# Optimization experiments

Hardware: AMD Instinct MI355X
Metric: run time of the kernel (lower is better)

The kernel has to match this reference:

```python
import jax, jax.numpy as jnp
import numpy as np
from math import sqrt

MASK_SCALE = 128  # band half-width; entries with |i-j| < MASK_SCALE are masked to -inf

B, L, H, E = 4, 2048, 8, 64
D = 64


def setup_inputs() -> dict:
    key = jax.random.key(0)
    kq, kk, kv = jax.random.split(key, 3)
    queries = jax.random.normal(kq, (B, L, H, E), dtype=jnp.float32)
    keys = jax.random.normal(kk, (B, L, H, E), dtype=jnp.float32)
    values = jax.random.normal(kv, (B, L, H, D), dtype=jnp.float32)
    attn_mask = jnp.zeros((B, 1, L, L), dtype=bool)  # unused (mask_flag=False)
    return {"queries": queries, "keys": keys, "values": values, "attn_mask": attn_mask}


def reference(queries, keys, values, attn_mask):
    b, l, h, e = queries.shape
    scale = 1.0 / sqrt(e)
    # [B,H,L,S] dense scores
    scores = jnp.einsum('blhe,bshe->bhls', queries, keys)
    # create_diag_symmetric_mask(L, MASK_SCALE): 1 iff |i-j| < MASK_SCALE
    idx = jnp.arange(l)
    band = jnp.abs(idx[:, None] - idx[None, :]) < MASK_SCALE  # [L,L]
    # module masks the band to -inf (attends outside the band)
    scores = jnp.where(band[None, None, :, :], -jnp.inf, scores)
    A = jax.nn.softmax(scale * scores, axis=-1)
    V = jnp.einsum('bhls,bshd->blhd', A, values)
    return V
```

## Files before the change

### kernel.cpp

```cpp
#include <hip/hip_runtime.h>
#include <hip/hip_bf16.h>

typedef __bf16 bf16_t;
typedef __bf16 bf16x8 __attribute__((ext_vector_type(8)));
typedef float f32x4 __attribute__((ext_vector_type(4)));
typedef float f32x16 __attribute__((ext_vector_type(16)));
typedef unsigned int u32;

#define MFMA16(A,B,C) __builtin_amdgcn_mfma_f32_16x16x32_bf16(A,B,C,0,0,0)
#define MFMA32(A,B,C) __builtin_amdgcn_mfma_f32_32x32x16_bf16(A,B,C,0,0,0)

constexpr int Bb = 4, Ll = 2048, Hh = 8, Ee = 64, Dd = 64;
constexpr int LDP = 72;
constexpr int MS = 128;

static __device__ __forceinline__ bf16x8 cvt8(float4 a, float4 b) {
    bf16x8 t;
    t[0] = (bf16_t)a.x; t[1] = (bf16_t)a.y; t[2] = (bf16_t)a.z; t[3] = (bf16_t)a.w;
    t[4] = (bf16_t)b.x; t[5] = (bf16_t)b.y; t[6] = (bf16_t)b.z; t[7] = (bf16_t)b.w;
    return t;
}

static __device__ __forceinline__ u32 pkbf(float lo, float hi) {
    u32 d;
    asm("v_cvt_pk_bf16_f32 %0, %1, %2" : "=v"(d) : "v"(lo), "v"(hi));
    return d;
}

static __device__ __forceinline__ float fexp2(float x) {
    float r;
    asm("v_exp_f32 %0, %1" : "=v"(r) : "v"(x));
    return r;
}

static __device__ __forceinline__ f32x16 zero16() {
    f32x16 z;
    #pragma unroll
    for (int r = 0; r < 16; ++r) z[r] = 0.f;
    return z;
}

__global__ __launch_bounds__(256) void prep(const float* __restrict__ K,
                                            const float* __restrict__ V,
                                            bf16_t* __restrict__ Kb,
                                            bf16_t* __restrict__ Vt) {
    __shared__ bf16_t VLp[Dd][LDP];
    if (blockIdx.x < 2048) {
        const int c = blockIdx.x * 256 + threadIdx.x;
        const int e0 = (c & 7) * 8;
        const int h  = (c >> 3) & (Hh - 1);
        const int l  = (c >> 6) & (Ll - 1);
        const int b  = c >> 17;
        const float* s = K + ((((size_t)b * Ll + l) * Hh + h) * Ee + e0);
        float4 f0 = ((const float4*)s)[0];
        float4 f1 = ((const float4*)s)[1];
        *(bf16x8*)(Kb + ((((size_t)b * Hh + h) * Ll + l) * Ee + e0)) = cvt8(f0, f1);
    } else {
        const int bb = blockIdx.x - 2048;
        const int bh = bb >> 5;
        const int t  = bb & 31;
        const int b = bh >> 3, h = bh & 7;
        {
            const int j  = threadIdx.x >> 2;
            const int d0 = (threadIdx.x & 3) * 16;
            const float* vp = V + (((size_t)(b * Ll + t * 64 + j)) * Hh + h) * Dd + d0;
            float4 x0 = ((const float4*)vp)[0], x1 = ((const float4*)vp)[1];
            float4 x2 = ((const float4*)vp)[2], x3 = ((const float4*)vp)[3];
            VLp[d0 +  0][j] = (bf16_t)x0.x; VLp[d0 +  1][j] = (bf16_t)x0.y;
            VLp[d0 +  2][j] = (bf16_t)x0.z; VLp[d0 +  3][j] = (bf16_t)x0.w;
            VLp[d0 +  4][j] = (bf16_t)x1.x; VLp[d0 +  5][j] = (bf16_t)x1.y;
            VLp[d0 +  6][j] = (bf16_t)x1.z; VLp[d0 +  7][j] = (bf16_t)x1.w;
            VLp[d0 +  8][j] = (bf16_t)x2.x; VLp[d0 +  9][j] = (bf16_t)x2.y;
            VLp[d0 + 10][j] = (bf16_t)x2.z; VLp[d0 + 11][j] = (bf16_t)x2.w;
            VLp[d0 + 12][j] = (bf16_t)x3.x; VLp[d0 + 13][j] = (bf16_t)x3.y;
            VLp[d0 + 14][j] = (bf16_t)x3.z; VLp[d0 + 15][j] = (bf16_t)x3.w;
        }
        __syncthreads();
        {
            const int d  = threadIdx.x >> 2;
            const int j0 = (threadIdx.x & 3) * 16;
            bf16x8 a0 = *(const bf16x8*)&VLp[d][j0];
            bf16x8 a1 = *(const bf16x8*)&VLp[d][j0 + 8];
            bf16_t* op = Vt + ((((size_t)bh * 32 + t) * 64 + d) * 64 + j0);
            *(bf16x8*)op = a0;
            *(bf16x8*)(op + 8) = a1;
        }
    }
}

__global__ __launch_bounds__(512, 1) void fattn10(const float* __restrict__ Q,
                                                  const bf16_t* __restrict__ Kb,
                                                  const bf16_t* __restrict__ Vt,
                                                  float* __restrict__ O) {
    __shared__ __align__(16) bf16_t KL[2 * 4096];
    __shared__ __align__(16) bf16_t VL[2 * 4096];

    const int tid = threadIdx.x;
    const int wv  = tid >> 6;
    const int ln  = tid & 63;
    const int l31 = ln & 31;
    const int lh  = ln >> 5;

    const int bid = blockIdx.x;
    const int x   = bid & 7;
    const int o   = bid >> 3;
    const int bh  = x * 4 + (o >> 3);
    const int p   = o & 7;
    const int qt  = (wv < 4) ? p : (p + 8);
    const int wq0 = qt * 128 + (wv & 3) * 32;
    const int qq  = wq0 + l31;
    const int b = bh >> 3, h = bh & 7;

    const bf16_t* kbase = Kb + (size_t)bh * (Ll * 64);
    const bf16_t* vbase = Vt + (size_t)bh * (Ll * 64);

    bf16x8 qreg[4];
    {
        const float SCL2 = 0.125f * 1.44269504f;
        const float* qp = Q + (((size_t)(b * Ll + qq)) * Hh + h) * Ee + lh * 8;
        #pragma unroll
        for (int ks = 0; ks < 4; ++ks) {
            float4 f0 = *(const float4*)(qp + ks * 16);
            float4 f1 = *(const float4*)(qp + ks * 16 + 4);
            f0.x *= SCL2; f0.y *= SCL2; f0.z *= SCL2; f0.w *= SCL2;
            f1.x *= SCL2; f1.y *= SCL2; f1.z *= SCL2; f1.w *= SCL2;
            qreg[ks] = cvt8(f0, f1);
        }
    }

    bf16x8 ones;
    #pragma unroll
    for (int e = 0; e < 8; ++e) ones[e] = (bf16_t)1.0f;

    f32x16 acc0 = zero16(), acc1 = zero16(), accP = zero16();

    const int srow = tid >> 3;
    const int soff = srow * 64 + (((tid & 7) ^ (srow & 7)) << 3);
    const int ldst = tid * 8;

    #define STAGE(nxt, kt_) do {                                                   \
        __builtin_amdgcn_global_load_lds((const void*)(kbase + (size_t)(kt_) * 4096\
                                         + soff), (void*)(KL + (nxt) * 4096 + ldst), 16, 0, 0); \
        __builtin_amdgcn_global_load_lds((const void*)(vbase + (size_t)(kt_) * 4096\
                                         + soff), (void*)(VL + (nxt) * 4096 + ldst), 16, 0, 0); \
    } while (0)

    STAGE(0, 0);

    for (int i = 0; i < 32; ++i) {
        const int k0 = i * 64;

        if (i + 1 < 32) {
            STAGE((i + 1) & 1, i + 1);
            asm volatile("s_waitcnt vmcnt(2)" ::: "memory");
        } else {
            asm volatile("s_waitcnt vmcnt(0)" ::: "memory");
        }
        __builtin_amdgcn_s_barrier();

        const int bo = (i & 1) * 4096;

        f32x16 s0v = zero16(), s1v = zero16();
        __builtin_amdgcn_s_setprio(1);
        #pragma unroll
        for (int ks = 0; ks < 4; ++ks) {
            const int cc = (((2 * ks + lh) ^ (l31 & 7)) << 3);
            bf16x8 ka0 = *(const bf16x8*)&KL[bo + l31 * 64 + cc];
            bf16x8 ka1 = *(const bf16x8*)&KL[bo + (32 + l31) * 64 + cc];
            s0v = MFMA32(ka0, qreg[ks], s0v);
            s1v = MFMA32(ka1, qreg[ks], s1v);
        }
        __builtin_amdgcn_s_setprio(0);

        {
            const int d0_ = wq0 - k0;
            if (d0_ > -159 && d0_ < 159) {
                #pragma unroll
                for (int r = 0; r < 16; ++r) {
                    const int k = k0 + 4 * lh + ((r & 3) + 8 * (r >> 2));
                    const int dlt = qq - k;
                    if (dlt > -MS && dlt < MS) s0v[r] = -1e30f;
                }
            }
            const int d1_ = wq0 - (k0 + 32);
            if (d1_ > -159 && d1_ < 159) {
                #pragma unroll
                for (int r = 0; r < 16; ++r) {
                    const int k = k0 + 32 + 4 * lh + ((r & 3) + 8 * (r >> 2));
                    const int dlt = qq - k;
                    if (dlt > -MS && dlt < MS) s1v[r] = -1e30f;
                }
            }
        }

        bf16x8 pf[4];
        {
            float pp[16];
            #pragma unroll
            for (int r = 0; r < 16; ++r) pp[r] = fexp2(s0v[r]);
            u32 x0 = pkbf(pp[0], pp[1]),   x1 = pkbf(pp[2], pp[3]);
            u32 x2 = pkbf(pp[4], pp[5]),   x3 = pkbf(pp[6], pp[7]);
            u32 x4 = pkbf(pp[8], pp[9]),   x5 = pkbf(pp[10], pp[11]);
            u32 x6 = pkbf(pp[12], pp[13]), x7 = pkbf(pp[14], pp[15]);
            asm volatile("v_permlane32_swap_b32 %0, %1" : "+v"(x0), "+v"(x2));
            asm volatile("v_permlane32_swap_b32 %0, %1" : "+v"(x1), "+v"(x3));
            asm volatile("v_permlane32_swap_b32 %0, %1" : "+v"(x4), "+v"(x6));
            asm volatile("v_permlane32_swap_b32 %0, %1" : "+v"(x5), "+v"(x7));
            union { u32 w[4]; bf16x8 v; } u0, u1;
            u0.w[0] = x0; u0.w[1] = x1; u0.w[2] = x2; u0.w[3] = x3;
            u1.w[0] = x4; u1.w[1] = x5; u1.w[2] = x6; u1.w[3] = x7;
            pf[0] = u0.v; pf[1] = u1.v;
        }
        {
            float pp[16];
            #pragma unroll
            for (int r = 0; r < 16; ++r) pp[r] = fexp2(s1v[r]);
            u32 x0 = pkbf(pp[0], pp[1]),   x1 = pkbf(pp[2], pp[3]);
            u32 x2 = pkbf(pp[4], pp[5]),   x3 = pkbf(pp[6], pp[7]);
            u32 x4 = pkbf(pp[8], pp[9]),   x5 = pkbf(pp[10], pp[11]);
            u32 x6 = pkbf(pp[12], pp[13]), x7 = pkbf(pp[14], pp[15]);
            asm volatile("v_permlane32_swap_b32 %0, %1" : "+v"(x0), "+v"(x2));
            asm volatile("v_permlane32_swap_b32 %0, %1" : "+v"(x1), "+v"(x3));
            asm volatile("v_permlane32_swap_b32 %0, %1" : "+v"(x4), "+v"(x6));
            asm volatile("v_permlane32_swap_b32 %0, %1" : "+v"(x5), "+v"(x7));
            union { u32 w[4]; bf16x8 v; } u0, u1;
            u0.w[0] = x0; u0.w[1] = x1; u0.w[2] = x2; u0.w[3] = x3;
            u1.w[0] = x4; u1.w[1] = x5; u1.w[2] = x6; u1.w[3] = x7;
            pf[2] = u0.v; pf[3] = u1.v;
        }

        __builtin_amdgcn_s_setprio(1);
        #pragma unroll
        for (int ks = 0; ks < 4; ++ks) {
            const int cc = (((2 * ks + lh) ^ (l31 & 7)) << 3);
            bf16x8 vf0 = *(const bf16x8*)&VL[bo + l31 * 64 + cc];
            bf16x8 vf1 = *(const bf16x8*)&VL[bo + (32 + l31) * 64 + cc];
            acc0 = MFMA32(pf[ks], vf0, acc0);
            acc1 = MFMA32(pf[ks], vf1, acc1);
            accP = MFMA32(pf[ks], ones, accP);
        }
        __builtin_amdgcn_s_setprio(0);

        __builtin_amdgcn_s_barrier();
    }
    #undef STAGE

    #pragma unroll
    for (int r = 0; r < 16; ++r) {
        const int rr = (r & 3) + 8 * (r >> 2) + 4 * lh;
        const float ir = 1.0f / accP[r];
        float* op = O + ((size_t)(b * Ll + wq0 + rr) * Hh + h) * Dd + l31;
        op[0]  = acc0[r] * ir;
        op[32] = acc1[r] * ir;
    }
}

__global__ __launch_bounds__(256, 2) void fattn_f32(const float* __restrict__ Q,
                                                    const float* __restrict__ K,
                                                    const float* __restrict__ V,
                                                    float* __restrict__ O) {
    __shared__ __align__(16) bf16_t Klds[64][LDP];
    __shared__ __align__(16) bf16_t Vtlds[Dd][LDP];
    __shared__ __align__(16) bf16_t Plds[4][16][LDP];

    const int tid = threadIdx.x;
    const int wv  = tid >> 6;
    const int ln  = tid & 63;
    const int l15 = ln & 15;
    const int g   = ln >> 4;

    const int nqt = Ll / 64;
    const int bid = blockIdx.x;
    const int qt  = bid % nqt;
    const int bh  = bid / nqt;
    const int b   = bh >> 3;
    const int h   = bh & 7;
    const int q0  = qt * 64;

    const float SCL2 = 0.125f * 1.44269504f;

    bf16x8 qf[2];
    {
        const float* qp = Q + (((size_t)(b * Ll + q0 + wv * 16 + l15)) * Hh + h) * Ee + g * 8;
        #pragma unroll
        for (int ks = 0; ks < 2; ++ks) {
            float4 f0 = *(const float4*)(qp + 32 * ks);
            float4 f1 = *(const float4*)(qp + 32 * ks + 4);
            qf[ks] = cvt8(f0, f1);
        }
    }

    f32x4 acc[4];
    #pragma unroll
    for (int ct = 0; ct < 4; ++ct) acc[ct] = (f32x4){0.f, 0.f, 0.f, 0.f};
    float m2[4], lsum[4];
    #pragma unroll
    for (int r = 0; r < 4; ++r) { m2[r] = -1e30f; lsum[r] = 0.f; }

    for (int k0 = 0; k0 < Ll; k0 += 64) {
        const int dd = k0 - q0;
        if (dd >= -64 && dd <= 64) continue;
        const bool needmask = (dd == 128) || (dd == -128);

        __syncthreads();
        {
            const int j  = tid >> 2;
            const int c0 = (tid & 3) << 4;
            const float* kp = K + (((size_t)(b * Ll + k0 + j)) * Hh + h) * Ee + c0;
            const float* vp = V + (((size_t)(b * Ll + k0 + j)) * Hh + h) * Dd + c0;
            float4 a0 = ((const float4*)kp)[0], a1 = ((const float4*)kp)[1];
            float4 a2 = ((const float4*)kp)[2], a3 = ((const float4*)kp)[3];
            *(bf16x8*)&Klds[j][c0]     = cvt8(a0, a1);
            *(bf16x8*)&Klds[j][c0 + 8] = cvt8(a2, a3);
            float4 b0 = ((const float4*)vp)[0], b1 = ((const float4*)vp)[1];
            float4 b2 = ((const float4*)vp)[2], b3 = ((const float4*)vp)[3];
            Vtlds[c0 +  0][j] = (bf16_t)b0.x; Vtlds[c0 +  1][j] = (bf16_t)b0.y;
            Vtlds[c0 +  2][j] = (bf16_t)b0.z; Vtlds[c0 +  3][j] = (bf16_t)b0.w;
            Vtlds[c0 +  4][j] = (bf16_t)b1.x; Vtlds[c0 +  5][j] = (bf16_t)b1.y;
            Vtlds[c0 +  6][j] = (bf16_t)b1.z; Vtlds[c0 +  7][j] = (bf16_t)b1.w;
            Vtlds[c0 +  8][j] = (bf16_t)b2.x; Vtlds[c0 +  9][j] = (bf16_t)b2.y;
            Vtlds[c0 + 10][j] = (bf16_t)b2.z; Vtlds[c0 + 11][j] = (bf16_t)b2.w;
            Vtlds[c0 + 12][j] = (bf16_t)b3.x; Vtlds[c0 + 13][j] = (bf16_t)b3.y;
            Vtlds[c0 + 14][j] = (bf16_t)b3.z; Vtlds[c0 + 15][j] = (bf16_t)b3.w;
        }
        __syncthreads();

        f32x4 s[4];
        #pragma unroll
        for (int ct = 0; ct < 4; ++ct) {
            f32x4 z = (f32x4){0.f, 0.f, 0.f, 0.f};
            #pragma unroll
            for (int ks = 0; ks < 2; ++ks) {
                bf16x8 kf = *(const bf16x8*)&Klds[ct * 16 + l15][ks * 32 + g * 8];
                z = MFMA16(qf[ks], kf, z);
            }
            s[ct] = z;
        }

        float lg[4][4];
        #pragma unroll
        for (int ct = 0; ct < 4; ++ct)
            #pragma unroll
            for (int r = 0; r < 4; ++r)
                lg[ct][r] = s[ct][r] * SCL2;

        if (needmask) {
            const int irow = q0 + wv * 16 + g * 4;
            #pragma unroll
            for (int ct = 0; ct < 4; ++ct) {
                const int j = k0 + ct * 16 + l15;
                #pragma unroll
                for (int r = 0; r < 4; ++r) {
                    int diff = irow + r - j;
                    diff = diff < 0 ? -diff : diff;
                    if (diff < MS) lg[ct][r] = -1e30f;
                }
            }
        }

        #pragma unroll
        for (int r = 0; r < 4; ++r) {
            float mx = fmaxf(fmaxf(lg[0][r], lg[1][r]), fmaxf(lg[2][r], lg[3][r]));
            #pragma unroll
            for (int off = 1; off < 16; off <<= 1) mx = fmaxf(mx, __shfl_xor(mx, off));
            const float mnew = fmaxf(m2[r], mx);
            const float c = exp2f(m2[r] - mnew);
            m2[r] = mnew;
            #pragma unroll
            for (int ct = 0; ct < 4; ++ct) acc[ct][r] *= c;
            float ps = 0.f;
            #pragma unroll
            for (int ct = 0; ct < 4; ++ct) {
                float p = exp2f(lg[ct][r] - mnew);
                bf16_t pb = (bf16_t)p;
                Plds[wv][g * 4 + r][ct * 16 + l15] = pb;
                ps += (float)pb;
            }
            #pragma unroll
            for (int off = 1; off < 16; off <<= 1) ps += __shfl_xor(ps, off);
            lsum[r] = lsum[r] * c + ps;
        }

        __syncthreads();

        #pragma unroll
        for (int ks = 0; ks < 2; ++ks) {
            bf16x8 pfr = *(const bf16x8*)&Plds[wv][l15][ks * 32 + g * 8];
            #pragma unroll
            for (int ct = 0; ct < 4; ++ct) {
                bf16x8 vfl = *(const bf16x8*)&Vtlds[ct * 16 + l15][ks * 32 + g * 8];
                acc[ct] = MFMA16(pfr, vfl, acc[ct]);
            }
        }
    }

    #pragma unroll
    for (int r = 0; r < 4; ++r) {
        const float inv = 1.0f / lsum[r];
        const size_t row = (size_t)(b * Ll + q0 + wv * 16 + g * 4 + r);
        float* op = O + (row * Hh + h) * Dd;
        #pragma unroll
        for (int ct = 0; ct < 4; ++ct)
            op[ct * 16 + l15] = acc[ct][r] * inv;
    }
}

extern "C" void kernel_launch(void* const* d_in, const int* in_sizes, int n_in,
                              void* d_out, int out_size, void* d_ws, size_t ws_size,
                              hipStream_t stream) {
    const float* Q = (const float*)d_in[0];
    const float* K = (const float*)d_in[1];
    const float* V = (const float*)d_in[2];
    float* O = (float*)d_out;

    const size_t nelem = (size_t)Bb * Hh * Ll * Ee;
    const size_t need  = nelem * 2 * 2;

    if (ws_size >= need) {
        bf16_t* Kb = (bf16_t*)d_ws;
        bf16_t* Vt = Kb + nelem;
        prep<<<dim3(3072), dim3(256), 0, stream>>>(K, V, Kb, Vt);
        fattn10<<<dim3(256), dim3(512), 0, stream>>>(Q, Kb, Vt, O);
    } else {
        fattn_f32<<<dim3(Bb * Hh * 32), dim3(256), 0, stream>>>(Q, K, V, O);
    }
}
```

Before: 63.34 us.

## Split key tiles across waves, skip fully masked tiles, reduce partials via LDS

The attention kernel is restructured into 1024 blocks of 256 threads, each owning a 64-query tile. The two wave pairs split each 64-key tile in half and merge their partial outputs and row sums through LDS at the end. Key tiles that fall entirely inside the masked band (up to three per query tile) are skipped. The ones-vector MFMA used for the row sum is replaced by a scalar sum plus a lane shuffle. This raises occupancy and cuts redundant work, at the cost of an extra LDS reduction and barriers.

```diff
diff --git a/kernel.cpp b/kernel.cpp
--- a/kernel.cpp
+++ b/kernel.cpp
@@ -88,33 +88,36 @@
     }
 }
 
-__global__ __launch_bounds__(512, 1) void fattn10(const float* __restrict__ Q,
+__global__ __launch_bounds__(256, 4) void fattn13(const float* __restrict__ Q,
                                                   const bf16_t* __restrict__ Kb,
                                                   const bf16_t* __restrict__ Vt,
                                                   float* __restrict__ O) {
-    __shared__ __align__(16) bf16_t KL[2 * 4096];
-    __shared__ __align__(16) bf16_t VL[2 * 4096];
+    __shared__ __align__(16) bf16_t SMEM[16384];
+    bf16_t* KL = SMEM;
+    bf16_t* VL = SMEM + 8192;
 
     const int tid = threadIdx.x;
     const int wv  = tid >> 6;
     const int ln  = tid & 63;
     const int l31 = ln & 31;
     const int lh  = ln >> 5;
+    const int khalf = wv & 1;
+    const int qhalf = wv >> 1;
 
     const int bid = blockIdx.x;
     const int x   = bid & 7;
     const int o   = bid >> 3;
-    const int bh  = x * 4 + (o >> 3);
-    const int p   = o & 7;
-    const int qt  = (wv < 4) ? p : (p + 8);
-    const int wq0 = qt * 128 + (wv & 3) * 32;
+    const int bh  = x * 4 + (o >> 5);
+    const int qt  = o & 31;
+    const int q0  = qt * 64;
+    const int wq0 = q0 + qhalf * 32;
     const int qq  = wq0 + l31;
     const int b = bh >> 3, h = bh & 7;
 
     const bf16_t* kbase = Kb + (size_t)bh * (Ll * 64);
     const bf16_t* vbase = Vt + (size_t)bh * (Ll * 64);
 
-    bf16x8 qreg[4];
+    bf16x8 qA[4];
     {
         const float SCL2 = 0.125f * 1.44269504f;
         const float* qp = Q + (((size_t)(b * Ll + qq)) * Hh + h) * Ee + lh * 8;
@@ -124,84 +127,85 @@
             float4 f1 = *(const float4*)(qp + ks * 16 + 4);
             f0.x *= SCL2; f0.y *= SCL2; f0.z *= SCL2; f0.w *= SCL2;
             f1.x *= SCL2; f1.y *= SCL2; f1.z *= SCL2; f1.w *= SCL2;
-            qreg[ks] = cvt8(f0, f1);
-        }
-    }
-
-    bf16x8 ones;
-    #pragma unroll
-    for (int e = 0; e < 8; ++e) ones[e] = (bf16_t)1.0f;
-
-    f32x16 acc0 = zero16(), acc1 = zero16(), accP = zero16();
-
-    const int srow = tid >> 3;
-    const int soff = srow * 64 + (((tid & 7) ^ (srow & 7)) << 3);
-    const int ldst = tid * 8;
+            qA[ks] = cvt8(f0, f1);
+        }
+    }
+
+    f32x16 acc0 = zero16(), acc1 = zero16();
+    float psum = 0.f;
+
+    const int rowoff = (ln >> 3) * 64 + (((ln & 7) ^ (ln >> 3)) * 8);
+    const int i0 = (wv & 1) * 4;
+    const bf16_t* gsb = (wv < 2) ? kbase : vbase;
+    bf16_t* lsb = (wv < 2) ? KL : VL;
+
+    const int sk0 = (qt > 0) ? (qt - 1) : 0;
+    const int skN = ((qt < 31) ? (qt + 1) : 31) - sk0 + 1;
+    const int NL  = 32 - skN;
+    #define TILEOF(i) (((i) < sk0) ? (i) : ((i) + skN))
 
     #define STAGE(nxt, kt_) do {                                                   \
-        __builtin_amdgcn_global_load_lds((const void*)(kbase + (size_t)(kt_) * 4096\
-                                         + soff), (void*)(KL + (nxt) * 4096 + ldst), 16, 0, 0); \
-        __builtin_amdgcn_global_load_lds((const void*)(vbase + (size_t)(kt_) * 4096\
-                                         + soff), (void*)(VL + (nxt) * 4096 + ldst), 16, 0, 0); \
+        const bf16_t* _g = gsb + (size_t)(kt_) * 4096 + i0 * 512 + rowoff;         \
+        bf16_t* _l = lsb + (nxt) * 4096 + i0 * 512;                                \
+        _Pragma("unroll")                                                          \
+        for (int _c = 0; _c < 4; ++_c)                                             \
+            __builtin_amdgcn_global_load_lds((const void*)(_g + _c * 512),         \
+                                             (void*)(_l + _c * 512), 16, 0, 0);    \
     } while (0)
 
-    STAGE(0, 0);
-
-    for (int i = 0; i < 32; ++i) {
-        const int k0 = i * 64;
-
-        if (i + 1 < 32) {
-            STAGE((i + 1) & 1, i + 1);
-            asm volatile("s_waitcnt vmcnt(2)" ::: "memory");
+    STAGE(0, TILEOF(0));
+
+    for (int i = 0; i < NL; ++i) {
+        const int kt_ = TILEOF(i);
+        const int k0 = kt_ * 64;
+        const int kk0 = k0 + khalf * 32;
+
+        if (i + 1 < NL) {
+            STAGE((i + 1) & 1, TILEOF(i + 1));
+            asm volatile("s_waitcnt vmcnt(4)" ::: "memory");
         } else {
             asm volatile("s_waitcnt vmcnt(0)" ::: "memory");
         }
         __builtin_amdgcn_s_barrier();
 
         const int bo = (i & 1) * 4096;
-
-        f32x16 s0v = zero16(), s1v = zero16();
+        const int krow = bo + khalf * 2048 + l31 * 64;
+
+        f32x16 sv = zero16();
         __builtin_amdgcn_s_setprio(1);
         #pragma unroll
         for (int ks = 0; ks < 4; ++ks) {
             const int cc = (((2 * ks + lh) ^ (l31 & 7)) << 3);
-            bf16x8 ka0 = *(const bf16x8*)&KL[bo + l31 * 64 + cc];
-            bf16x8 ka1 = *(const bf16x8*)&KL[bo + (32 + l31) * 64 + cc];
-            s0v = MFMA32(ka0, qreg[ks], s0v);
-            s1v = MFMA32(ka1, qreg[ks], s1v);
+            bf16x8 ka = *(const bf16x8*)&KL[krow + cc];
+            sv = MFMA32(ka, qA[ks], sv);
         }
         __builtin_amdgcn_s_setprio(0);
 
         {
-            const int d0_ = wq0 - k0;
-            if (d0_ > -159 && d0_ < 159) {
+            const int dw = wq0 - kk0;
+            if (dw > -159 && dw < 159) {
                 #pragma unroll
                 for (int r = 0; r < 16; ++r) {
-                    const int k = k0 + 4 * lh + ((r & 3) + 8 * (r >> 2));
+                    const int k = kk0 + 4 * lh + ((r & 3) + 8 * (r >> 2));
                     const int dlt = qq - k;
-                    if (dlt > -MS && dlt < MS) s0v[r] = -1e30f;
+                    if (dlt > -MS && dlt < MS) sv[r] = -1e30f;
                 }
             }
-            const int d1_ = wq0 - (k0 + 32);
-            if (d1_ > -159 && d1_ < 159) {
-                #pragma unroll
-                for (int r = 0; r < 16; ++r) {
-                    const int k = k0 + 32 + 4 * lh + ((r & 3) + 8 * (r >> 2));
-                    const int dlt = qq - k;
-                    if (dlt > -MS && dlt < MS) s1v[r] = -1e30f;
-                }
-            }
-        }
-
-        bf16x8 pf[4];
+        }
+
+        bf16x8 pf0, pf1;
         {
-            float pp[16];
-            #pragma unroll
-            for (int r = 0; r < 16; ++r) pp[r] = fexp2(s0v[r]);
-            u32 x0 = pkbf(pp[0], pp[1]),   x1 = pkbf(pp[2], pp[3]);
-            u32 x2 = pkbf(pp[4], pp[5]),   x3 = pkbf(pp[6], pp[7]);
-            u32 x4 = pkbf(pp[8], pp[9]),   x5 = pkbf(pp[10], pp[11]);
-            u32 x6 = pkbf(pp[12], pp[13]), x7 = pkbf(pp[14], pp[15]);
+            float p[16];
+            #pragma unroll
+            for (int r = 0; r < 16; ++r) p[r] = fexp2(sv[r]);
+            psum += (((p[0] + p[1]) + (p[2] + p[3])) +
+                     ((p[4] + p[5]) + (p[6] + p[7]))) +
+                    (((p[8] + p[9]) + (p[10] + p[11])) +
+                     ((p[12] + p[13]) + (p[14] + p[15])));
+            u32 x0 = pkbf(p[0], p[1]),   x1 = pkbf(p[2], p[3]);
+            u32 x2 = pkbf(p[4], p[5]),   x3 = pkbf(p[6], p[7]);
+            u32 x4 = pkbf(p[8], p[9]),   x5 = pkbf(p[10], p[11]);
+            u32 x6 = pkbf(p[12], p[13]), x7 = pkbf(p[14], p[15]);
             asm volatile("v_permlane32_swap_b32 %0, %1" : "+v"(x0), "+v"(x2));
             asm volatile("v_permlane32_swap_b32 %0, %1" : "+v"(x1), "+v"(x3));
             asm volatile("v_permlane32_swap_b32 %0, %1" : "+v"(x4), "+v"(x6));
@@ -209,49 +213,56 @@
             union { u32 w[4]; bf16x8 v; } u0, u1;
             u0.w[0] = x0; u0.w[1] = x1; u0.w[2] = x2; u0.w[3] = x3;
             u1.w[0] = x4; u1.w[1] = x5; u1.w[2] = x6; u1.w[3] = x7;
-            pf[0] = u0.v; pf[1] = u1.v;
-        }
-        {
-            float pp[16];
-            #pragma unroll
-            for (int r = 0; r < 16; ++r) pp[r] = fexp2(s1v[r]);
-            u32 x0 = pkbf(pp[0], pp[1]),   x1 = pkbf(pp[2], pp[3]);
-            u32 x2 = pkbf(pp[4], pp[5]),   x3 = pkbf(pp[6], pp[7]);
-            u32 x4 = pkbf(pp[8], pp[9]),   x5 = pkbf(pp[10], pp[11]);
-            u32 x6 = pkbf(pp[12], pp[13]), x7 = pkbf(pp[14], pp[15]);
-            asm volatile("v_permlane32_swap_b32 %0, %1" : "+v"(x0), "+v"(x2));
-            asm volatile("v_permlane32_swap_b32 %0, %1" : "+v"(x1), "+v"(x3));
-            asm volatile("v_permlane32_swap_b32 %0, %1" : "+v"(x4), "+v"(x6));
-            asm volatile("v_permlane32_swap_b32 %0, %1" : "+v"(x5), "+v"(x7));
-            union { u32 w[4]; bf16x8 v; } u0, u1;
-            u0.w[0] = x0; u0.w[1] = x1; u0.w[2] = x2; u0.w[3] = x3;
-            u1.w[0] = x4; u1.w[1] = x5; u1.w[2] = x6; u1.w[3] = x7;
-            pf[2] = u0.v; pf[3] = u1.v;
+            pf0 = u0.v; pf1 = u1.v;
         }
 
         __builtin_amdgcn_s_setprio(1);
         #pragma unroll
-        for (int ks = 0; ks < 4; ++ks) {
-            const int cc = (((2 * ks + lh) ^ (l31 & 7)) << 3);
+        for (int t = 0; t < 2; ++t) {
+            const int cc = (((4 * khalf + 2 * t + lh) ^ (l31 & 7)) << 3);
             bf16x8 vf0 = *(const bf16x8*)&VL[bo + l31 * 64 + cc];
             bf16x8 vf1 = *(const bf16x8*)&VL[bo + (32 + l31) * 64 + cc];
-            acc0 = MFMA32(pf[ks], vf0, acc0);
-            acc1 = MFMA32(pf[ks], vf1, acc1);
-            accP = MFMA32(pf[ks], ones, accP);
+            bf16x8 pa = t ? pf1 : pf0;
+            acc0 = MFMA32(pa, vf0, acc0);
+            acc1 = MFMA32(pa, vf1, acc1);
         }
         __builtin_amdgcn_s_setprio(0);
 
         __builtin_amdgcn_s_barrier();
     }
     #undef STAGE
-
-    #pragma unroll
-    for (int r = 0; r < 16; ++r) {
-        const int rr = (r & 3) + 8 * (r >> 2) + 4 * lh;
-        const float ir = 1.0f / accP[r];
-        float* op = O + ((size_t)(b * Ll + wq0 + rr) * Hh + h) * Dd + l31;
-        op[0]  = acc0[r] * ir;
-        op[32] = acc1[r] * ir;
+    #undef TILEOF
+
+    psum += __shfl_xor(psum, 32);
+    __syncthreads();
+    float* LF = (float*)SMEM;
+    const int mb = qhalf * 33 * 64;
+
+    if (khalf == 1) {
+        #pragma unroll
+        for (int r = 0; r < 16; ++r) {
+            LF[mb + r * 64 + ln]        = acc0[r];
+            LF[mb + (16 + r) * 64 + ln] = acc1[r];
+        }
+        LF[mb + 32 * 64 + ln] = psum;
+    }
+    __syncthreads();
+    if (khalf == 0) {
+        #pragma unroll
+        for (int r = 0; r < 16; ++r) {
+            acc0[r] += LF[mb + r * 64 + ln];
+            acc1[r] += LF[mb + (16 + r) * 64 + ln];
+        }
+        psum += LF[mb + 32 * 64 + ln];
+        const float inv = 1.0f / psum;
+        #pragma unroll
+        for (int r = 0; r < 16; ++r) {
+            const int rr = (r & 3) + 8 * (r >> 2) + 4 * lh;
+            const float ir = __shfl(inv, rr);
+            float* op = O + ((size_t)(b * Ll + wq0 + rr) * Hh + h) * Dd + l31;
+            op[0]  = acc0[r] * ir;
+            op[32] = acc1[r] * ir;
+        }
     }
 }
 
@@ -420,7 +431,7 @@
         bf16_t* Kb = (bf16_t*)d_ws;
         bf16_t* Vt = Kb + nelem;
         prep<<<dim3(3072), dim3(256), 0, stream>>>(K, V, Kb, Vt);
-        fattn10<<<dim3(256), dim3(512), 0, stream>>>(Q, Kb, Vt, O);
+        fattn13<<<dim3(1024), dim3(256), 0, stream>>>(Q, Kb, Vt, O);
     } else {
         fattn_f32<<<dim3(Bb * Hh * 32), dim3(256), 0, stream>>>(Q, K, V, O);
     }
```

Measured after the change: 59.88 us. -5.5%, faster.
